# Performance work log

Measured on AMD Instinct MI355X. Metric: run time of the kernel, lower is better.

Reference implementation:

```python
import jax, jax.numpy as jnp
import numpy as np

H = 128
STEPS = 4
EPS = 1e-5

def _mlp(x, W0, b0, W1, b1, W2, b2):
    x = jax.nn.relu(x @ W0 + b0)
    x = jax.nn.relu(x @ W1 + b1)
    return x @ W2 + b2

def _ln(x, g, b):
    mu = jnp.mean(x, axis=-1, keepdims=True)
    var = jnp.mean((x - mu) ** 2, axis=-1, keepdims=True)
    return (x - mu) * jax.lax.rsqrt(var + EPS) * g + b

def _scores(x, pos):
    # soft assignment of points to graph nodes: softmax over -squared distance
    d2 = (jnp.sum(x * x, -1, keepdims=True)
          - 2.0 * jnp.einsum('bnd,md->bnm', x, pos)
          + jnp.sum(pos * pos, -1))  # [B, Npts, Nnodes]
    return jax.nn.softmax(-d2, axis=-1)

def _block(nodes, senders, receivers, msg_W, msg_b, ln1_g, ln1_b, node_W, node_b, ln2_g, ln2_b):
    # gather edge endpoints, message MLP, layernorm
    m = jnp.concatenate((nodes[:, receivers], nodes[:, senders]), axis=-1) @ msg_W + msg_b
    m = _ln(m, ln1_g, ln1_b)  # [B, E, H]
    inbox = jnp.zeros_like(nodes).at[:, receivers].add(m)  # scatter-add
    out = jnp.concatenate((nodes, inbox), axis=-1) @ node_W + node_b
    return _ln(out, ln2_g, ln2_b)

def setup_inputs() -> dict:
    key = jax.random.key(0)
    ks = jax.random.split(key, 40)
    B, Nc, Nt, N, E = 8, 4096, 4096, 1024, 16384
    dx, dyc, dyt = 2, 3, 3
    def w(k, *s):
        fan_in = s[0]
        return jax.random.normal(k, s, jnp.float32) / np.sqrt(fan_in)
    inp = {
        'xc': jax.random.normal(ks[0], (B, Nc, dx), jnp.float32),
        'yc': jax.random.normal(ks[1], (B, Nc, dyc), jnp.float32),
        'xt': jax.random.normal(ks[2], (B, Nt, dx), jnp.float32),
        'pos': jax.random.normal(ks[3], (N, dx), jnp.float32),
        'enc_W0': w(ks[4], dx + dyc, H), 'enc_b0': jnp.zeros((H,), jnp.float32),
        'enc_W1': w(ks[5], H, H), 'enc_b1': jnp.zeros((H,), jnp.float32),
        'enc_W2': w(ks[6], H, H), 'enc_b2': jnp.zeros((H,), jnp.float32),
        'qenc_W0': w(ks[7], dx, H), 'qenc_b0': jnp.zeros((H,), jnp.float32),
        'qenc_W1': w(ks[8], H, H), 'qenc_b1': jnp.zeros((H,), jnp.float32),
        'qenc_W2': w(ks[9], H, H), 'qenc_b2': jnp.zeros((H,), jnp.float32),
        'dec_W0': w(ks[10], 2 * H, H), 'dec_b0': jnp.zeros((H,), jnp.float32),
        'dec_W1': w(ks[11], H, H), 'dec_b1': jnp.zeros((H,), jnp.float32),
        'dec_W2': w(ks[12], H, dyt), 'dec_b2': jnp.zeros((dyt,), jnp.float32),
        'msg_W': w(ks[13], 2 * H, H), 'msg_b': jnp.zeros((H,), jnp.float32),
        'ln1_g': jnp.ones((H,), jnp.float32), 'ln1_b': jnp.zeros((H,), jnp.float32),
        'node_W': w(ks[14], 2 * H, H), 'node_b': jnp.zeros((H,), jnp.float32),
        'ln2_g': jnp.ones((H,), jnp.float32), 'ln2_b': jnp.zeros((H,), jnp.float32),
        'senders': jax.random.randint(ks[15], (E,), 0, N, jnp.int32),
        'receivers': jax.random.randint(ks[16], (E,), 0, N, jnp.int32),
    }
    return inp

def reference(xc, yc, xt, pos,
              enc_W0, enc_b0, enc_W1, enc_b1, enc_W2, enc_b2,
              qenc_W0, qenc_b0, qenc_W1, qenc_b1, qenc_W2, qenc_b2,
              dec_W0, dec_b0, dec_W1, dec_b1, dec_W2, dec_b2,
              msg_W, msg_b, ln1_g, ln1_b, node_W, node_b, ln2_g, ln2_b,
              senders, receivers):
    sc = _scores(xc, pos)  # [B, Nc, N]
    emb = _mlp(jnp.concatenate((xc, yc), -1), enc_W0, enc_b0, enc_W1, enc_b1, enc_W2, enc_b2)
    latents = jnp.einsum('bcn,bch->bnh', sc, emb)  # scores^T @ emb -> [B, N, H]
    for _ in range(STEPS):  # shared block (same weights each step)
        latents = _block(latents, senders, receivers, msg_W, msg_b, ln1_g, ln1_b,
                         node_W, node_b, ln2_g, ln2_b)
    q = _mlp(xt, qenc_W0, qenc_b0, qenc_W1, qenc_b1, qenc_W2, qenc_b2)
    st = _scores(xt, pos)  # [B, Nt, N]
    z = jnp.einsum('btn,bnh->bth', st, latents)
    z = jnp.concatenate((z, q), -1)
    return _mlp(z, dec_W0, dec_b0, dec_W1, dec_b1, dec_W2, dec_b2)
```

## Files before the change

### kernel.cpp

```cpp
#include <hip/hip_runtime.h>
#include <hip/hip_bf16.h>
#include <string.h>

#define BB 8
#define NC 4096
#define NTT 4096
#define NNODE 1024
#define NEDGE 16384
#define LDE 4128
#define LDL 1056

typedef __hip_bfloat16 bf16;
typedef unsigned short u16;
typedef __attribute__((ext_vector_type(8))) short short8;
typedef __attribute__((ext_vector_type(4))) float f32x4;

__device__ __forceinline__ float b2f(bf16 x) { return __bfloat162float(x); }
__device__ __forceinline__ float bs2f(short s) { return __uint_as_float(((unsigned)(unsigned short)s) << 16); }

template <typename T> struct Cvt;
template <> struct Cvt<float> { static __device__ __forceinline__ float to(float v) { return v; } };
template <> struct Cvt<bf16>  { static __device__ __forceinline__ bf16  to(float v) { return __float2bfloat16(v); } };

__device__ __forceinline__ unsigned short f2bs(float x) {
    unsigned u = __float_as_uint(x);
    return (unsigned short)((u + 0x7FFFu + ((u >> 16) & 1u)) >> 16);
}

__device__ __forceinline__ short8 ld_frag(const bf16* g) {
    union { uint4 u4; short8 s8; } cv;
    cv.u4 = *(const uint4*)g;
    return cv.s8;
}
__device__ __forceinline__ short8 ld_frag(const float* g) {
    float4 f0 = *(const float4*)g;
    float4 f1 = *(const float4*)(g + 4);
    short8 r;
    r[0] = (short)f2bs(f0.x); r[1] = (short)f2bs(f0.y);
    r[2] = (short)f2bs(f0.z); r[3] = (short)f2bs(f0.w);
    r[4] = (short)f2bs(f1.x); r[5] = (short)f2bs(f1.y);
    r[6] = (short)f2bs(f1.z); r[7] = (short)f2bs(f1.w);
    return r;
}

__global__ void detect_k(const u16* __restrict__ posu, int* __restrict__ flag) {
    __shared__ int cnt;
    if (threadIdx.x == 0) cnt = 0;
    __syncthreads();
    int wild = 0;
    for (int i = threadIdx.x; i < 1024; i += 256) {
        u16 u = posu[2 * i];
        int ex = (u >> 7) & 0xFF;
        if (ex == 0 || ex == 0xFF || ex > 137 || ex < 107) wild++;
    }
    atomicAdd(&cnt, wild);
    __syncthreads();
    if (threadIdx.x == 0) *flag = (cnt > 50) ? 1 : 0;
}

struct Tab { const void* src[30]; int pref[31]; };

__global__ __launch_bounds__(256) void ingest_k(Tab tab, const int* __restrict__ flag,
                                                bf16* __restrict__ dst) {
    int idx = blockIdx.x * 256 + threadIdx.x;
    if (idx >= tab.pref[30]) return;
    int t = 0;
    while (tab.pref[t + 1] <= idx) t++;
    int e = idx - tab.pref[t];
    float v;
    if (*flag) v = ((const float*)tab.src[t])[e];
    else       v = b2f(((const bf16*)tab.src[t])[e]);
    dst[idx] = __float2bfloat16(v);
}

struct TT { const bf16* src[11]; bf16* dst[11]; int srcK[11]; int dK[11]; int pref[12]; };

__global__ __launch_bounds__(256) void prep_trans_k(
    TT tt,
    const bf16* __restrict__ xc, const bf16* __restrict__ yc,
    const bf16* __restrict__ xt,
    const bf16* __restrict__ pos,
    bf16* __restrict__ xin32, bf16* __restrict__ xt32,
    float2* __restrict__ posf2) {
    if (blockIdx.x < 128) {
        int row = blockIdx.x * 256 + threadIdx.x;
        bf16 z = __float2bfloat16(0.f);
        bf16* xr = xin32 + row * 32;
        xr[0] = xc[row * 2 + 0];
        xr[1] = xc[row * 2 + 1];
        xr[2] = yc[row * 3 + 0];
        xr[3] = yc[row * 3 + 1];
        xr[4] = yc[row * 3 + 2];
#pragma unroll
        for (int k = 5; k < 32; ++k) xr[k] = z;
        bf16* tr = xt32 + row * 32;
        tr[0] = xt[row * 2 + 0];
        tr[1] = xt[row * 2 + 1];
#pragma unroll
        for (int k = 2; k < 32; ++k) tr[k] = z;
        if (row < NNODE) posf2[row] = make_float2(b2f(pos[2 * row]), b2f(pos[2 * row + 1]));
        return;
    }
    int idx = (blockIdx.x - 128) * 256 + threadIdx.x;
    if (idx >= tt.pref[11]) return;
    int t = 0;
    while (tt.pref[t + 1] <= idx) t++;
    int e = idx - tt.pref[t];
    int k = e >> 7, n = e & 127;
    bf16 v = (k < tt.srcK[t]) ? tt.src[t][k * 128 + n] : __float2bfloat16(0.f);
    tt.dst[t][n * tt.dK[t] + k] = v;
}

__global__ __launch_bounds__(1024) void build_csr_k(const int* __restrict__ recv,
                                                    const int* __restrict__ send,
                                                    int* __restrict__ rowptr,
                                                    int* __restrict__ csr_send) {
    __shared__ int cnt[1024];
    __shared__ int wt[16], wt2[16];
    __shared__ int cur[1024];
    int t = threadIdx.x;
    cnt[t] = 0;
    __syncthreads();
    for (int e = t; e < NEDGE; e += 1024) atomicAdd(&cnt[recv[e]], 1);
    __syncthreads();
    int v = cnt[t];
    int lane = t & 63, w = t >> 6;
#pragma unroll
    for (int off = 1; off < 64; off <<= 1) {
        int u = __shfl_up(v, off);
        if (lane >= off) v += u;
    }
    if (lane == 63) wt[w] = v;
    __syncthreads();
    if (t < 16) {
        int x = wt[t];
#pragma unroll
        for (int off = 1; off < 16; off <<= 1) {
            int u = __shfl_up(x, off);
            if (t >= off) x += u;
        }
        wt2[t] = x;
    }
    __syncthreads();
    int excl = v - cnt[t] + (w ? wt2[w - 1] : 0);
    rowptr[t] = excl;
    cur[t] = excl;
    if (t == 0) rowptr[1024] = NEDGE;
    __syncthreads();
    for (int e = t; e < NEDGE; e += 1024) {
        int pos = atomicAdd(&cur[recv[e]], 1);
        csr_send[pos] = send[e];
    }
}

template <int KSTEPS, int EPI, int RELU, int TRANS, int NSPLIT,
          typename TINA, typename TINB, typename TOUT>
__global__ __launch_bounds__(256) void mfma_gemm_k(
    const TINA* __restrict__ Xa, const TINB* __restrict__ Xb, int ldx,
    const bf16* __restrict__ Wt,
    const bf16* __restrict__ bias,
    const bf16* __restrict__ lng, const bf16* __restrict__ lnb,
    TOUT* __restrict__ Y, int ldy, int tshift, int ldt)
{
    constexpr int K = KSTEPS * 32;
    __shared__ __align__(16) short Bs[8][64][8];
    int tid = threadIdx.x;
    int w = tid >> 6, l = tid & 63;
    int lm = l & 15, lq = l >> 4;
    int blk = blockIdx.x;
    int half = 0;
    if (NSPLIT == 2) { half = blk & 1; blk >>= 1; }
    const bf16* Wtl = Wt + (size_t)half * 128 * K;
    int colbase = half * 128;
    size_t row0 = (size_t)blk * 64;

    f32x4 acc[8];
#pragma unroll
    for (int i = 0; i < 8; i++) acc[i] = (f32x4){0.f, 0.f, 0.f, 0.f};

    for (int s = 0; s < KSTEPS; ++s) {
        int k0 = s * 32;
        __syncthreads();
        short8 a;
        if (Xb != nullptr && k0 >= 128)
            a = ld_frag(Xb + (row0 + w * 16 + lm) * (size_t)128 + (k0 - 128) + lq * 8);
        else
            a = ld_frag(Xa + (row0 + w * 16 + lm) * (size_t)ldx + k0 + lq * 8);
#pragma unroll
        for (int rr = 0; rr < 2; ++rr) {
            int idx = rr * 256 + tid;
            int nt = idx >> 6, ll = idx & 63;
            *(short8*)&Bs[nt][ll][0] =
                ld_frag(Wtl + (size_t)(nt * 16 + (ll & 15)) * K + k0 + (ll >> 4) * 8);
        }
        __syncthreads();
#pragma unroll
        for (int nt = 0; nt < 8; ++nt) {
            short8 b = *(const short8*)&Bs[nt][l][0];
            acc[nt] = __builtin_amdgcn_mfma_f32_16x16x32_bf16(a, b, acc[nt], 0, 0, 0);
        }
    }

    float v[8][4];
#pragma unroll
    for (int nt = 0; nt < 8; ++nt) {
        float bb = bias ? b2f(bias[colbase + nt * 16 + lm]) : 0.f;
#pragma unroll
        for (int r = 0; r < 4; ++r) v[nt][r] = acc[nt][r] + bb;
    }
    if constexpr (EPI == 1) {
#pragma unroll
        for (int r = 0; r < 4; ++r) {
            float s1 = 0.f, s2 = 0.f;
#pragma unroll
            for (int nt = 0; nt < 8; ++nt) { s1 += v[nt][r]; s2 += v[nt][r] * v[nt][r]; }
#pragma unroll
            for (int m = 1; m < 16; m <<= 1) { s1 += __shfl_xor(s1, m); s2 += __shfl_xor(s2, m); }
            float mu = s1 * (1.f / 128.f);
            float var = s2 * (1.f / 128.f) - mu * mu;
            float rs = rsqrtf(var + 1e-5f);
#pragma unroll
            for (int nt = 0; nt < 8; ++nt) {
                int n = nt * 16 + lm;
                v[nt][r] = (v[nt][r] - mu) * rs * b2f(lng[n]) + b2f(lnb[n]);
            }
        }
    }
    if constexpr (TRANS) {
        size_t grow = row0 + w * 16 + lq * 4;
        int bb2 = (int)(grow >> tshift);
        size_t rloc = grow & (((size_t)1 << tshift) - 1);
        bf16* YT = (bf16*)Y;
#pragma unroll
        for (int nt = 0; nt < 8; ++nt) {
            int col = colbase + nt * 16 + lm;
            ushort4 u;
            float x0 = v[nt][0], x1 = v[nt][1], x2 = v[nt][2], x3 = v[nt][3];
            if (RELU) { x0 = fmaxf(x0, 0.f); x1 = fmaxf(x1, 0.f); x2 = fmaxf(x2, 0.f); x3 = fmaxf(x3, 0.f); }
            u.x = f2bs(x0); u.y = f2bs(x1); u.z = f2bs(x2); u.w = f2bs(x3);
            *(ushort4*)(YT + ((size_t)bb2 * 128 + col) * (size_t)ldt + rloc) = u;
        }
    } else {
#pragma unroll
        for (int nt = 0; nt < 8; ++nt)
#pragma unroll
            for (int r = 0; r < 4; ++r) {
                float x = v[nt][r];
                if (RELU) x = fmaxf(x, 0.f);
                Y[(row0 + w * 16 + lq * 4 + r) * (size_t)ldy + colbase + nt * 16 + lm] = Cvt<TOUT>::to(x);
            }
    }
}

__global__ __launch_bounds__(256) void node_msg_k(
    const float* __restrict__ cur, const bf16* __restrict__ inbox,
    const bf16* __restrict__ WtNode, const bf16* __restrict__ node_b,
    const bf16* __restrict__ ln2_g, const bf16* __restrict__ ln2_b,
    const bf16* __restrict__ WtMsg,
    float* __restrict__ nxt, bf16* __restrict__ PQ)
{
    __shared__ __align__(16) short Bs[8][64][8];
    __shared__ __align__(16) short Act[64][136];
    int tid = threadIdx.x;
    int w = tid >> 6, l = tid & 63;
    int lm = l & 15, lq = l >> 4;
    size_t row0 = (size_t)blockIdx.x * 64;

    f32x4 acc[8];
#pragma unroll
    for (int i = 0; i < 8; i++) acc[i] = (f32x4){0.f, 0.f, 0.f, 0.f};

    for (int s = 0; s < 8; ++s) {
        int k0 = s * 32;
        __syncthreads();
        short8 a;
        if (k0 < 128) a = ld_frag(cur + (row0 + w * 16 + lm) * 128 + k0 + lq * 8);
        else          a = ld_frag(inbox + (row0 + w * 16 + lm) * 128 + (k0 - 128) + lq * 8);
#pragma unroll
        for (int rr = 0; rr < 2; ++rr) {
            int idx = rr * 256 + tid;
            int nt = idx >> 6, ll = idx & 63;
            *(short8*)&Bs[nt][ll][0] =
                ld_frag(WtNode + (size_t)(nt * 16 + (ll & 15)) * 256 + k0 + (ll >> 4) * 8);
        }
        __syncthreads();
#pragma unroll
        for (int nt = 0; nt < 8; ++nt) {
            short8 b = *(const short8*)&Bs[nt][l][0];
            acc[nt] = __builtin_amdgcn_mfma_f32_16x16x32_bf16(a, b, acc[nt], 0, 0, 0);
        }
    }
    float v[8][4];
#pragma unroll
    for (int nt = 0; nt < 8; ++nt) {
        float bb = b2f(node_b[nt * 16 + lm]);
#pragma unroll
        for (int r = 0; r < 4; ++r) v[nt][r] = acc[nt][r] + bb;
    }
#pragma unroll
    for (int r = 0; r < 4; ++r) {
        float s1 = 0.f, s2 = 0.f;
#pragma unroll
        for (int nt = 0; nt < 8; ++nt) { s1 += v[nt][r]; s2 += v[nt][r] * v[nt][r]; }
#pragma unroll
        for (int m = 1; m < 16; m <<= 1) { s1 += __shfl_xor(s1, m); s2 += __shfl_xor(s2, m); }
        float mu = s1 * (1.f / 128.f);
        float var = s2 * (1.f / 128.f) - mu * mu;
        float rs = rsqrtf(var + 1e-5f);
#pragma unroll
        for (int nt = 0; nt < 8; ++nt) {
            int n = nt * 16 + lm;
            v[nt][r] = (v[nt][r] - mu) * rs * b2f(ln2_g[n]) + b2f(ln2_b[n]);
        }
    }
#pragma unroll
    for (int nt = 0; nt < 8; ++nt)
#pragma unroll
        for (int r = 0; r < 4; ++r) {
            nxt[(row0 + w * 16 + lq * 4 + r) * 128 + nt * 16 + lm] = v[nt][r];
            Act[w * 16 + lq * 4 + r][nt * 16 + lm] = (short)f2bs(v[nt][r]);
        }

    for (int half = 0; half < 2; ++half) {
        const bf16* Wtl = WtMsg + (size_t)half * 128 * 128;
#pragma unroll
        for (int i = 0; i < 8; i++) acc[i] = (f32x4){0.f, 0.f, 0.f, 0.f};
        for (int s = 0; s < 4; ++s) {
            int k0 = s * 32;
            __syncthreads();
#pragma unroll
            for (int rr = 0; rr < 2; ++rr) {
                int idx = rr * 256 + tid;
                int nt = idx >> 6, ll = idx & 63;
                *(short8*)&Bs[nt][ll][0] =
                    ld_frag(Wtl + (size_t)(nt * 16 + (ll & 15)) * 128 + k0 + (ll >> 4) * 8);
            }
            __syncthreads();
            short8 a = *(const short8*)&Act[w * 16 + lm][k0 + lq * 8];
#pragma unroll
            for (int nt = 0; nt < 8; ++nt) {
                short8 b = *(const short8*)&Bs[nt][l][0];
                acc[nt] = __builtin_amdgcn_mfma_f32_16x16x32_bf16(a, b, acc[nt], 0, 0, 0);
            }
        }
#pragma unroll
        for (int nt = 0; nt < 8; ++nt)
#pragma unroll
            for (int r = 0; r < 4; ++r)
                PQ[(row0 + w * 16 + lq * 4 + r) * 256 + half * 128 + nt * 16 + lm] =
                    __float2bfloat16(acc[nt][r]);
    }
}

template <int K0STEPS, int LAYERS, int RELU_LAST, int TRANS, typename TIN, typename TOUT>
__global__ __launch_bounds__(256) void mlp_k(
    const TIN* __restrict__ Xa, const TIN* __restrict__ Xb, int ldx,
    const bf16* __restrict__ Wt0, const bf16* __restrict__ b0,
    const bf16* __restrict__ Wt1, const bf16* __restrict__ b1,
    const bf16* __restrict__ Wt2, const bf16* __restrict__ b2,
    TOUT* __restrict__ Y, int ldy, int tshift, int ldt)
{
    constexpr int K0 = K0STEPS * 32;
    __shared__ __align__(16) short Bs[8][64][8];
    __shared__ __align__(16) short Act[64][136];
    int tid = threadIdx.x;
    int w = tid >> 6, l = tid & 63;
    int lm = l & 15, lq = l >> 4;
    size_t row0 = (size_t)blockIdx.x * 64;

    f32x4 acc[8];
#pragma unroll
    for (int i = 0; i < 8; i++) acc[i] = (f32x4){0.f, 0.f, 0.f, 0.f};

    for (int s = 0; s < K0STEPS; ++s) {
        int k0 = s * 32;
        __syncthreads();
        short8 a;
        {
            const TIN* src = Xa; int kk = k0; int ld = ldx;
            if (Xb != nullptr && k0 >= 128) { src = Xb; kk = k0 - 128; ld = 128; }
            a = ld_frag(src + (row0 + w * 16 + lm) * (size_t)ld + kk + lq * 8);
        }
#pragma unroll
        for (int rr = 0; rr < 2; ++rr) {
            int idx = rr * 256 + tid;
            int nt = idx >> 6, ll = idx & 63;
            *(short8*)&Bs[nt][ll][0] =
                ld_frag(Wt0 + (size_t)(nt * 16 + (ll & 15)) * K0 + k0 + (ll >> 4) * 8);
        }
        __syncthreads();
#pragma unroll
        for (int nt = 0; nt < 8; ++nt) {
            short8 b = *(const short8*)&Bs[nt][l][0];
            acc[nt] = __builtin_amdgcn_mfma_f32_16x16x32_bf16(a, b, acc[nt], 0, 0, 0);
        }
    }
#pragma unroll
    for (int nt = 0; nt < 8; ++nt) {
        float bb = b2f(b0[nt * 16 + lm]);
#pragma unroll
        for (int r = 0; r < 4; ++r) {
            float x = fmaxf(acc[nt][r] + bb, 0.f);
            Act[w * 16 + lq * 4 + r][nt * 16 + lm] = (short)f2bs(x);
        }
    }

    for (int L = 1; L < LAYERS; ++L) {
        const bf16* Wt = (L == 1) ? Wt1 : Wt2;
        const bf16* bias = (L == 1) ? b1 : b2;
        bool last = (L == LAYERS - 1);
#pragma unroll
        for (int i = 0; i < 8; i++) acc[i] = (f32x4){0.f, 0.f, 0.f, 0.f};
        for (int s = 0; s < 4; ++s) {
            int k0 = s * 32;
            __syncthreads();
#pragma unroll
            for (int rr = 0; rr < 2; ++rr) {
                int idx = rr * 256 + tid;
                int nt = idx >> 6, ll = idx & 63;
                *(short8*)&Bs[nt][ll][0] =
                    ld_frag(Wt + (size_t)(nt * 16 + (ll & 15)) * 128 + k0 + (ll >> 4) * 8);
            }
            __syncthreads();
            short8 a = *(const short8*)&Act[w * 16 + lm][k0 + lq * 8];
#pragma unroll
            for (int nt = 0; nt < 8; ++nt) {
                short8 b = *(const short8*)&Bs[nt][l][0];
                acc[nt] = __builtin_amdgcn_mfma_f32_16x16x32_bf16(a, b, acc[nt], 0, 0, 0);
            }
        }
        if (!last) {
            __syncthreads();
#pragma unroll
            for (int nt = 0; nt < 8; ++nt) {
                float bb = b2f(bias[nt * 16 + lm]);
#pragma unroll
                for (int r = 0; r < 4; ++r) {
                    float x = fmaxf(acc[nt][r] + bb, 0.f);
                    Act[w * 16 + lq * 4 + r][nt * 16 + lm] = (short)f2bs(x);
                }
            }
        } else {
            float v[8][4];
#pragma unroll
            for (int nt = 0; nt < 8; ++nt) {
                float bb = b2f(bias[nt * 16 + lm]);
#pragma unroll
                for (int r = 0; r < 4; ++r) {
                    float x = acc[nt][r] + bb;
                    if (RELU_LAST) x = fmaxf(x, 0.f);
                    v[nt][r] = x;
                }
            }
            if constexpr (TRANS) {
                size_t grow = row0 + w * 16 + lq * 4;
                int bb2 = (int)(grow >> tshift);
                size_t rloc = grow & (((size_t)1 << tshift) - 1);
                bf16* YT = (bf16*)Y;
#pragma unroll
                for (int nt = 0; nt < 8; ++nt) {
                    int col = nt * 16 + lm;
                    ushort4 u;
                    u.x = f2bs(v[nt][0]); u.y = f2bs(v[nt][1]);
                    u.z = f2bs(v[nt][2]); u.w = f2bs(v[nt][3]);
                    *(ushort4*)(YT + ((size_t)bb2 * 128 + col) * (size_t)ldt + rloc) = u;
                }
            } else {
#pragma unroll
                for (int nt = 0; nt < 8; ++nt)
#pragma unroll
                    for (int r = 0; r < 4; ++r)
                        Y[(row0 + w * 16 + lq * 4 + r) * (size_t)ldy + nt * 16 + lm] =
                            Cvt<TOUT>::to(v[nt][r]);
            }
        }
    }
}

__global__ __launch_bounds__(256) void qdec_k(
    const bf16* __restrict__ xt32,
    const bf16* __restrict__ WtQ0, const bf16* __restrict__ qb0,
    const bf16* __restrict__ WtQ1, const bf16* __restrict__ qb1,
    const bf16* __restrict__ WtQ2, const bf16* __restrict__ qb2,
    const bf16* __restrict__ z,
    const bf16* __restrict__ WtDec0, const bf16* __restrict__ db0,
    const bf16* __restrict__ WtDec1, const bf16* __restrict__ db1,
    const bf16* __restrict__ W2, const bf16* __restrict__ b2v,
    const int* __restrict__ flag, void* __restrict__ out)
{
    __shared__ __align__(16) short Bs[8][64][8];
    __shared__ __align__(16) short Act[64][136];
    __shared__ bf16 w2s[384];
    int tid = threadIdx.x;
    int w = tid >> 6, l = tid & 63;
    int lm = l & 15, lq = l >> 4;
    size_t row0 = (size_t)blockIdx.x * 64;
    for (int t = tid; t < 384; t += 256) w2s[t] = W2[t];

    f32x4 acc[8];
#pragma unroll
    for (int i = 0; i < 8; i++) acc[i] = (f32x4){0.f, 0.f, 0.f, 0.f};

    {
        __syncthreads();
#pragma unroll
        for (int rr = 0; rr < 2; ++rr) {
            int idx = rr * 256 + tid;
            int nt = idx >> 6, ll = idx & 63;
            *(short8*)&Bs[nt][ll][0] =
                ld_frag(WtQ0 + (size_t)(nt * 16 + (ll & 15)) * 32 + (ll >> 4) * 8);
        }
        __syncthreads();
        short8 a = ld_frag(xt32 + (row0 + w * 16 + lm) * 32 + lq * 8);
#pragma unroll
        for (int nt = 0; nt < 8; ++nt) {
            short8 b = *(const short8*)&Bs[nt][l][0];
            acc[nt] = __builtin_amdgcn_mfma_f32_16x16x32_bf16(a, b, acc[nt], 0, 0, 0);
        }
#pragma unroll
        for (int nt = 0; nt < 8; ++nt) {
            float bb = b2f(qb0[nt * 16 + lm]);
#pragma unroll
            for (int r = 0; r < 4; ++r)
                Act[w * 16 + lq * 4 + r][nt * 16 + lm] = (short)f2bs(fmaxf(acc[nt][r] + bb, 0.f));
        }
    }
    for (int L = 1; L < 3; ++L) {
        const bf16* Wt = (L == 1) ? WtQ1 : WtQ2;
        const bf16* bias = (L == 1) ? qb1 : qb2;
#pragma unroll
        for (int i = 0; i < 8; i++) acc[i] = (f32x4){0.f, 0.f, 0.f, 0.f};
        for (int s = 0; s < 4; ++s) {
            int k0 = s * 32;
            __syncthreads();
#pragma unroll
            for (int rr = 0; rr < 2; ++rr) {
                int idx = rr * 256 + tid;
                int nt = idx >> 6, ll = idx & 63;
                *(short8*)&Bs[nt][ll][0] =
                    ld_frag(Wt + (size_t)(nt * 16 + (ll & 15)) * 128 + k0 + (ll >> 4) * 8);
            }
            __syncthreads();
            short8 a = *(const short8*)&Act[w * 16 + lm][k0 + lq * 8];
#pragma unroll
            for (int nt = 0; nt < 8; ++nt) {
                short8 b = *(const short8*)&Bs[nt][l][0];
                acc[nt] = __builtin_amdgcn_mfma_f32_16x16x32_bf16(a, b, acc[nt], 0, 0, 0);
            }
        }
        __syncthreads();
#pragma unroll
        for (int nt = 0; nt < 8; ++nt) {
            float bb = b2f(bias[nt * 16 + lm]);
#pragma unroll
            for (int r = 0; r < 4; ++r) {
                float x = acc[nt][r] + bb;
                if (L == 1) x = fmaxf(x, 0.f);
                Act[w * 16 + lq * 4 + r][nt * 16 + lm] = (short)f2bs(x);
            }
        }
    }
    {
#pragma unroll
        for (int i = 0; i < 8; i++) acc[i] = (f32x4){0.f, 0.f, 0.f, 0.f};
        for (int s = 0; s < 8; ++s) {
            int k0 = s * 32;
            __syncthreads();
#pragma unroll
            for (int rr = 0; rr < 2; ++rr) {
                int idx = rr * 256 + tid;
                int nt = idx >> 6, ll = idx & 63;
                *(short8*)&Bs[nt][ll][0] =
                    ld_frag(WtDec0 + (size_t)(nt * 16 + (ll & 15)) * 256 + k0 + (ll >> 4) * 8);
            }
            __syncthreads();
            short8 a;
            if (k0 < 128) a = ld_frag(z + (row0 + w * 16 + lm) * (size_t)128 + k0 + lq * 8);
            else          a = *(const short8*)&Act[w * 16 + lm][(k0 - 128) + lq * 8];
#pragma unroll
            for (int nt = 0; nt < 8; ++nt) {
                short8 b = *(const short8*)&Bs[nt][l][0];
                acc[nt] = __builtin_amdgcn_mfma_f32_16x16x32_bf16(a, b, acc[nt], 0, 0, 0);
            }
        }
        __syncthreads();
#pragma unroll
        for (int nt = 0; nt < 8; ++nt) {
            float bb = b2f(db0[nt * 16 + lm]);
#pragma unroll
            for (int r = 0; r < 4; ++r)
                Act[w * 16 + lq * 4 + r][nt * 16 + lm] = (short)f2bs(fmaxf(acc[nt][r] + bb, 0.f));
        }
    }
    {
#pragma unroll
        for (int i = 0; i < 8; i++) acc[i] = (f32x4){0.f, 0.f, 0.f, 0.f};
        for (int s = 0; s < 4; ++s) {
            int k0 = s * 32;
            __syncthreads();
#pragma unroll
            for (int rr = 0; rr < 2; ++rr) {
                int idx = rr * 256 + tid;
                int nt = idx >> 6, ll = idx & 63;
                *(short8*)&Bs[nt][ll][0] =
                    ld_frag(WtDec1 + (size_t)(nt * 16 + (ll & 15)) * 128 + k0 + (ll >> 4) * 8);
            }
            __syncthreads();
            short8 a = *(const short8*)&Act[w * 16 + lm][k0 + lq * 8];
#pragma unroll
            for (int nt = 0; nt < 8; ++nt) {
                short8 b = *(const short8*)&Bs[nt][l][0];
                acc[nt] = __builtin_amdgcn_mfma_f32_16x16x32_bf16(a, b, acc[nt], 0, 0, 0);
            }
        }
        __syncthreads();
#pragma unroll
        for (int nt = 0; nt < 8; ++nt) {
            float bb = b2f(db1[nt * 16 + lm]);
#pragma unroll
            for (int r = 0; r < 4; ++r)
                Act[w * 16 + lq * 4 + r][nt * 16 + lm] = (short)f2bs(fmaxf(acc[nt][r] + bb, 0.f));
        }
    }
    __syncthreads();
    if (tid < 192) {
        int row = tid / 3, col = tid - (tid / 3) * 3;
        float a = b2f(b2v[col]);
        for (int k8 = 0; k8 < 16; ++k8) {
            short8 av = *(const short8*)&Act[row][k8 * 8];
#pragma unroll
            for (int j = 0; j < 8; ++j)
                a += bs2f(av[j]) * b2f(w2s[(k8 * 8 + j) * 3 + col]);
        }
        size_t o = (row0 + row) * 3 + col;
        if (*flag) ((float*)out)[o] = a;
        else       ((bf16*)out)[o] = __float2bfloat16(a);
    }
}

__global__ __launch_bounds__(256) void stats2_k(const bf16* __restrict__ xcp,
                                                const bf16* __restrict__ xtp,
                                                const bf16* __restrict__ pos,
                                                float4* __restrict__ cstC4,
                                                float4* __restrict__ cstT4) {
    __shared__ float px[NNODE], py[NNODE];
    int tid = threadIdx.x;
    for (int t = tid; t < NNODE; t += 256) {
        px[t] = b2f(pos[2 * t]);
        py[t] = b2f(pos[2 * t + 1]);
    }
    __syncthreads();
    const bf16* xp = (blockIdx.x < 8192) ? xcp : xtp;
    float4* st4 = (blockIdx.x < 8192) ? cstC4 : cstT4;
    int pb = blockIdx.x & 8191;
    int w = tid >> 6, l = tid & 63;
    int p = pb * 4 + w;
    float x = b2f(xp[2 * p]), y = b2f(xp[2 * p + 1]);
    float vals[16];
    float m = -3.4e38f;
#pragma unroll
    for (int k = 0; k < 16; k++) {
        int n = k * 64 + l;
        float dx = x - px[n], dy = y - py[n];
        float v = -(dx * dx + dy * dy);
        vals[k] = v;
        m = fmaxf(m, v);
    }
#pragma unroll
    for (int off = 32; off; off >>= 1) m = fmaxf(m, __shfl_xor(m, off));
    float s = 0.f;
#pragma unroll
    for (int k = 0; k < 16; k++) s += __expf(vals[k] - m);
#pragma unroll
    for (int off = 32; off; off >>= 1) s += __shfl_xor(s, off);
    if (l == 0) st4[p] = make_float4(x, y, m, 1.f / s);
}

struct P8 { float* p[8]; };

__global__ __launch_bounds__(512, 4) void lat_mfma_k(const bf16* __restrict__ embT,
                                                     const float2* __restrict__ posf2,
                                                     const float4* __restrict__ cstC4,
                                                     P8 parts) {
    int i = blockIdx.x;
    int b = i & 7, r = i >> 3;
    int cs = r >> 4, nt = r & 15;
    int n0 = nt * 64;
    __shared__ __align__(16) float4 csh[512];
    __shared__ __align__(16) float4 red[4][8][64];
    int tid = threadIdx.x;
    int w = tid >> 6, l = tid & 63;
    int wl = w & 3, up = w >> 2;
    int lm = l & 15, lq = l >> 4;
    int node = n0 + wl * 16 + lm;
    float2 pn = posf2[node];
    const bf16* ebase = embT + (size_t)b * (128 * LDE) + cs * 512;
    const float4* cbase = cstC4 + b * NC + cs * 512;
    for (int t = tid; t < 512; t += 512) csh[t] = cbase[t];
    __syncthreads();

    f32x4 acc[8];
#pragma unroll
    for (int q = 0; q < 8; q++) acc[q] = (f32x4){0.f, 0.f, 0.f, 0.f};

    union AF { short8 s; u16 u[8]; };
    AF cw, nw;
    short8 bc[8], bn[8];
    int chb = up * 8;
    int c00 = chb * 32;
#pragma unroll
    for (int j = 0; j < 8; ++j) {
        float4 cc = csh[c00 + lq * 8 + j];
        float dx = cc.x - pn.x, dy = cc.y - pn.y;
        cw.u[j] = f2bs(__expf(-(dx * dx + dy * dy) - cc.z) * cc.w);
    }
#pragma unroll
    for (int t2 = 0; t2 < 8; ++t2)
        bc[t2] = ld_frag(ebase + (size_t)(t2 * 16 + lm) * LDE + c00 + lq * 8);

    for (int ch = 0; ch < 8; ++ch) {
        int c0n = (chb + ((ch + 1) & 7)) * 32;
#pragma unroll
        for (int t2 = 0; t2 < 8; ++t2)
            bn[t2] = ld_frag(ebase + (size_t)(t2 * 16 + lm) * LDE + c0n + lq * 8);
#pragma unroll
        for (int j = 0; j < 8; ++j) {
            float4 cc = csh[c0n + lq * 8 + j];
            float dx = cc.x - pn.x, dy = cc.y - pn.y;
            nw.u[j] = f2bs(__expf(-(dx * dx + dy * dy) - cc.z) * cc.w);
        }
#pragma unroll
        for (int t2 = 0; t2 < 8; ++t2)
            acc[t2] = __builtin_amdgcn_mfma_f32_16x16x32_bf16(cw.s, bc[t2], acc[t2], 0, 0, 0);
        cw = nw;
#pragma unroll
        for (int t2 = 0; t2 < 8; ++t2) bc[t2] = bn[t2];
    }
    if (up) {
#pragma unroll
        for (int t2 = 0; t2 < 8; ++t2)
            red[wl][t2][l] = make_float4(acc[t2][0], acc[t2][1], acc[t2][2], acc[t2][3]);
    }
    __syncthreads();
    if (!up) {
        float* part = parts.p[cs] + (((size_t)(b * NNODE + n0 + wl * 16 + lq * 4)) << 7) + lm;
#pragma unroll
        for (int t2 = 0; t2 < 8; ++t2) {
            float4 o = red[wl][t2][l];
#pragma unroll
            for (int r2 = 0; r2 < 4; ++r2)
                part[(r2 << 7) + t2 * 16] = acc[t2][r2] + ((const float*)&o)[r2];
        }
    }
}

__global__ __launch_bounds__(256) void reduce8_k(float* __restrict__ dst, P8 parts) {
    int i = blockIdx.x * 256 + threadIdx.x;
    float4 s = ((const float4*)parts.p[0])[i];
#pragma unroll
    for (int k = 1; k < 8; ++k) {
        float4 v = ((const float4*)parts.p[k])[i];
        s.x += v.x; s.y += v.y; s.z += v.z; s.w += v.w;
    }
    ((float4*)dst)[i] = s;
}

__global__ __launch_bounds__(512, 4) void z_mfma_k(const bf16* __restrict__ latT,
                                                   const float2* __restrict__ posf2,
                                                   const float4* __restrict__ cstT4,
                                                   bf16* __restrict__ z) {
    int i = blockIdx.x;
    int b = i & 7, tt = i >> 3;
    int t0 = tt * 64;
    __shared__ __align__(8) float2 posh[1024];
    __shared__ __align__(16) float4 red[4][8][64];
    int tid = threadIdx.x;
    int w = tid >> 6, l = tid & 63;
    int wl = w & 3, up = w >> 2;
    int lm = l & 15, lq = l >> 4;
    int t = t0 + wl * 16 + lm;
    float4 qs = cstT4[b * NTT + t];
    const bf16* lbase = latT + (size_t)b * (128 * LDL);
    for (int k = tid; k < 1024; k += 512) posh[k] = posf2[k];
    __syncthreads();

    f32x4 acc[8];
#pragma unroll
    for (int q = 0; q < 8; q++) acc[q] = (f32x4){0.f, 0.f, 0.f, 0.f};

    union AF { short8 s; u16 u[8]; };
    AF cw, nw;
    short8 bc[8], bn[8];
    int chb = up * 16;
    int nb0 = chb * 32;
#pragma unroll
    for (int j = 0; j < 8; ++j) {
        float2 pn = posh[nb0 + lq * 8 + j];
        float dx = qs.x - pn.x, dy = qs.y - pn.y;
        cw.u[j] = f2bs(__expf(-(dx * dx + dy * dy) - qs.z) * qs.w);
    }
#pragma unroll
    for (int t2 = 0; t2 < 8; ++t2)
        bc[t2] = ld_frag(lbase + (size_t)(t2 * 16 + lm) * LDL + nb0 + lq * 8);

    for (int ch = 0; ch < 16; ++ch) {
        int nbn = (chb + ((ch + 1) & 15)) * 32;
#pragma unroll
        for (int t2 = 0; t2 < 8; ++t2)
            bn[t2] = ld_frag(lbase + (size_t)(t2 * 16 + lm) * LDL + nbn + lq * 8);
#pragma unroll
        for (int j = 0; j < 8; ++j) {
            float2 pn = posh[nbn + lq * 8 + j];
            float dx = qs.x - pn.x, dy = qs.y - pn.y;
            nw.u[j] = f2bs(__expf(-(dx * dx + dy * dy) - qs.z) * qs.w);
        }
#pragma unroll
        for (int t2 = 0; t2 < 8; ++t2)
            acc[t2] = __builtin_amdgcn_mfma_f32_16x16x32_bf16(cw.s, bc[t2], acc[t2], 0, 0, 0);
        cw = nw;
#pragma unroll
        for (int t2 = 0; t2 < 8; ++t2) bc[t2] = bn[t2];
    }
    if (up) {
#pragma unroll
        for (int t2 = 0; t2 < 8; ++t2)
            red[wl][t2][l] = make_float4(acc[t2][0], acc[t2][1], acc[t2][2], acc[t2][3]);
    }
    __syncthreads();
    if (!up) {
        bf16* zp = z + (((size_t)(b * NTT + t0 + wl * 16 + lq * 4)) << 7) + lm;
#pragma unroll
        for (int t2 = 0; t2 < 8; ++t2) {
            float4 o = red[wl][t2][l];
#pragma unroll
            for (int r2 = 0; r2 < 4; ++r2)
                zp[(r2 << 7) + t2 * 16] = __float2bfloat16(acc[t2][r2] + ((const float*)&o)[r2]);
        }
    }
}

__global__ __launch_bounds__(256) void edge_gather_k(const bf16* __restrict__ PQ,
                                                     const int* __restrict__ rowptr,
                                                     const int* __restrict__ csr_send,
                                                     const bf16* __restrict__ mb,
                                                     const bf16* __restrict__ g1,
                                                     const bf16* __restrict__ b1,
                                                     bf16* __restrict__ inbox) {
    int tid = threadIdx.x;
    int w = tid >> 6, l = tid & 63;
    int gw = blockIdx.x * 4 + w;
    int b = gw >> 10, n = gw & 1023;
    const bf16* pqb = PQ + ((size_t)b << 18);
    float p0 = b2f(pqb[(n << 8) + l]);
    float p1 = b2f(pqb[(n << 8) + l + 64]);
    float mb0 = b2f(mb[l]), mb1 = b2f(mb[l + 64]);
    float g0 = b2f(g1[l]), g1v = b2f(g1[l + 64]);
    float bb0 = b2f(b1[l]), bb1 = b2f(b1[l + 64]);
    int beg = rowptr[n], end = rowptr[n + 1];
    float a0 = 0.f, a1 = 0.f;
    int i = beg;
    for (; i + 1 < end; i += 2) {
        int sA = csr_send[i], sB = csr_send[i + 1];
        const bf16* qA = pqb + (sA << 8) + 128;
        const bf16* qB = pqb + (sB << 8) + 128;
        float A0 = p0 + b2f(qA[l]) + mb0;
        float A1 = p1 + b2f(qA[l + 64]) + mb1;
        float B0 = p0 + b2f(qB[l]) + mb0;
        float B1 = p1 + b2f(qB[l + 64]) + mb1;
        float a1s = A0 + A1, a2s = A0 * A0 + A1 * A1;
        float b1s = B0 + B1, b2s = B0 * B0 + B1 * B1;
#pragma unroll
        for (int off = 32; off; off >>= 1) {
            a1s += __shfl_xor(a1s, off);
            a2s += __shfl_xor(a2s, off);
            b1s += __shfl_xor(b1s, off);
            b2s += __shfl_xor(b2s, off);
        }
        float muA = a1s * (1.f / 128.f);
        float varA = a2s * (1.f / 128.f) - muA * muA;
        float rsA = rsqrtf(varA + 1e-5f);
        float muB = b1s * (1.f / 128.f);
        float varB = b2s * (1.f / 128.f) - muB * muB;
        float rsB = rsqrtf(varB + 1e-5f);
        a0 += (A0 - muA) * rsA * g0 + bb0;
        a1 += (A1 - muA) * rsA * g1v + bb1;
        a0 += (B0 - muB) * rsB * g0 + bb0;
        a1 += (B1 - muB) * rsB * g1v + bb1;
    }
    if (i < end) {
        int s = csr_send[i];
        const bf16* q = pqb + (s << 8) + 128;
        float m0 = p0 + b2f(q[l]) + mb0;
        float m1 = p1 + b2f(q[l + 64]) + mb1;
        float s1 = m0 + m1, s2 = m0 * m0 + m1 * m1;
#pragma unroll
        for (int off = 32; off; off >>= 1) {
            s1 += __shfl_xor(s1, off);
            s2 += __shfl_xor(s2, off);
        }
        float mu = s1 * (1.f / 128.f);
        float var = s2 * (1.f / 128.f) - mu * mu;
        float rs = rsqrtf(var + 1e-5f);
        a0 += (m0 - mu) * rs * g0 + bb0;
        a1 += (m1 - mu) * rs * g1v + bb1;
    }
    bf16* inb = inbox + ((size_t)b << 17) + (n << 7);
    inb[l] = __float2bfloat16(a0);
    inb[l + 64] = __float2bfloat16(a1);
}

extern "C" void kernel_launch(void* const* d_in, const int* in_sizes, int n_in,
                              void* d_out, int out_size, void* d_ws, size_t ws_size,
                              hipStream_t stream) {
    const int* senders = (const int*)d_in[30];
    const int* receivers = (const int*)d_in[31];

    char* base = (char*)d_ws;
    size_t off = 0;
    auto alloc = [&](size_t bytes) { char* p = base + off; off += (bytes + 255) & ~(size_t)255; return p; };

    int* flag = (int*)alloc(256);

    Tab tab;
    int pref = 0;
    for (int i = 0; i < 30; ++i) { tab.src[i] = d_in[i]; tab.pref[i] = pref; pref += in_sizes[i]; }
    tab.pref[30] = pref;
    bf16* arena = (bf16*)alloc((size_t)pref * 2);
    auto C = [&](int i) { return arena + tab.pref[i]; };

    float4* cstC4 = (float4*)alloc(32768 * sizeof(float4));
    float4* cstT4 = (float4*)alloc(32768 * sizeof(float4));
    float* lat0  = (float*)alloc(8192 * 128 * 4);
    float* lat1  = (float*)alloc(8192 * 128 * 4);
    float* inboxf = (float*)alloc(8192 * 128 * 4);
    bf16* inbox  = (bf16*)alloc(8192 * 128 * 2);
    bf16* T1     = (bf16*)alloc((size_t)32768 * 128 * 2);
    bf16* T2     = (bf16*)alloc((size_t)32768 * 128 * 2);
    bf16* T3     = (bf16*)alloc((size_t)32768 * 128 * 2);
    bf16* embT   = (bf16*)alloc((size_t)8 * 128 * LDE * 2);
    bf16* latT   = (bf16*)alloc((size_t)8 * 128 * LDL * 2);
    bf16* xin32  = (bf16*)alloc((size_t)32768 * 32 * 2);
    bf16* xt32   = (bf16*)alloc((size_t)32768 * 32 * 2);
    float2* posf2 = (float2*)alloc(1024 * sizeof(float2));
    int* rowptr  = (int*)alloc(1025 * 4);
    int* csr_send = (int*)alloc(NEDGE * 4);
    bf16* WtEnc0 = (bf16*)alloc(128 * 32 * 2);
    bf16* WtQ0   = (bf16*)alloc(128 * 32 * 2);
    bf16* WtEnc1 = (bf16*)alloc(16384 * 2);
    bf16* WtEnc2 = (bf16*)alloc(16384 * 2);
    bf16* WtQ1   = (bf16*)alloc(16384 * 2);
    bf16* WtQ2   = (bf16*)alloc(16384 * 2);
    bf16* WtDec0 = (bf16*)alloc(32768 * 2);
    bf16* WtDec1 = (bf16*)alloc(16384 * 2);
    bf16* WtMsg  = (bf16*)alloc(32768 * 2);
    bf16* WtNode = (bf16*)alloc(32768 * 2);
    bf16* PQ     = T3;
    (void)ws_size; (void)n_in; (void)out_size;

    detect_k<<<1, 256, 0, stream>>>((const u16*)d_in[3], flag);
    ingest_k<<<(pref + 255) / 256, 256, 0, stream>>>(tab, flag, arena);

    const bf16 *xc = C(0), *yc = C(1), *xt = C(2), *pos = C(3);
    const bf16 *enc_W0 = C(4), *enc_b0 = C(5), *enc_W1 = C(6), *enc_b1 = C(7), *enc_W2 = C(8), *enc_b2 = C(9);
    const bf16 *qenc_W0 = C(10), *qenc_b0 = C(11), *qenc_W1 = C(12), *qenc_b1 = C(13), *qenc_W2 = C(14), *qenc_b2 = C(15);
    const bf16 *dec_W0 = C(16), *dec_b0 = C(17), *dec_W1 = C(18), *dec_b1 = C(19), *dec_W2 = C(20), *dec_b2 = C(21);
    const bf16 *msg_W = C(22), *msg_b = C(23), *ln1_g = C(24), *ln1_b = C(25);
    const bf16 *node_W = C(26), *node_b = C(27), *ln2_g = C(28), *ln2_b = C(29);

    TT tt;
    const bf16* s11[11] = { enc_W1, enc_W2, qenc_W1, qenc_W2, dec_W1, dec_W0, msg_W, msg_W + 16384, node_W, enc_W0, qenc_W0 };
    bf16* d11[11]       = { WtEnc1, WtEnc2, WtQ1,    WtQ2,    WtDec1, WtDec0, WtMsg, WtMsg + 16384, WtNode, WtEnc0, WtQ0   };
    int sk11[11] = { 128, 128, 128, 128, 128, 256, 128, 128, 256, 5, 2 };
    int dk11[11] = { 128, 128, 128, 128, 128, 256, 128, 128, 256, 32, 32 };
    int tp = 0;
    for (int i = 0; i < 11; ++i) {
        tt.src[i] = s11[i]; tt.dst[i] = d11[i]; tt.srcK[i] = sk11[i]; tt.dK[i] = dk11[i];
        tt.pref[i] = tp; tp += dk11[i] * 128;
    }
    tt.pref[11] = tp;

    prep_trans_k<<<128 + (tp + 255) / 256, 256, 0, stream>>>(tt, xc, yc, xt, pos, xin32, xt32, posf2);
    build_csr_k<<<1, 1024, 0, stream>>>(receivers, senders, rowptr, csr_send);

    mlp_k<1, 3, 0, 1, bf16, bf16><<<512, 256, 0, stream>>>(
        xin32, nullptr, 32, WtEnc0, enc_b0, WtEnc1, enc_b1, WtEnc2, enc_b2, embT, 128, 12, LDE);

    stats2_k<<<16384, 256, 0, stream>>>(xc, xt, pos, cstC4, cstT4);

    P8 parts;
    parts.p[0] = lat1;
    parts.p[1] = inboxf;
    parts.p[2] = (float*)T1;
    parts.p[3] = (float*)T1 + 1048576;
    parts.p[4] = (float*)T2;
    parts.p[5] = (float*)T2 + 1048576;
    parts.p[6] = (float*)T3;
    parts.p[7] = (float*)T3 + 1048576;
    lat_mfma_k<<<1024, 512, 0, stream>>>(embT, posf2, cstC4, parts);
    reduce8_k<<<1024, 256, 0, stream>>>(lat0, parts);

    mfma_gemm_k<4, 0, 0, 0, 2, float, float, bf16><<<256, 256, 0, stream>>>(lat0, nullptr, 128, WtMsg, nullptr, nullptr, nullptr, PQ, 256, 0, 0);
    edge_gather_k<<<2048, 256, 0, stream>>>(PQ, rowptr, csr_send, msg_b, ln1_g, ln1_b, inbox);
    node_msg_k<<<128, 256, 0, stream>>>(lat0, inbox, WtNode, node_b, ln2_g, ln2_b, WtMsg, lat1, PQ);
    edge_gather_k<<<2048, 256, 0, stream>>>(PQ, rowptr, csr_send, msg_b, ln1_g, ln1_b, inbox);
    node_msg_k<<<128, 256, 0, stream>>>(lat1, inbox, WtNode, node_b, ln2_g, ln2_b, WtMsg, lat0, PQ);
    edge_gather_k<<<2048, 256, 0, stream>>>(PQ, rowptr, csr_send, msg_b, ln1_g, ln1_b, inbox);
    node_msg_k<<<128, 256, 0, stream>>>(lat0, inbox, WtNode, node_b, ln2_g, ln2_b, WtMsg, lat1, PQ);
    edge_gather_k<<<2048, 256, 0, stream>>>(PQ, rowptr, csr_send, msg_b, ln1_g, ln1_b, inbox);
    mfma_gemm_k<8, 1, 0, 1, 1, float, bf16, bf16><<<128, 256, 0, stream>>>(lat1, inbox, 128, WtNode, node_b, ln2_g, ln2_b, latT, 128, 10, LDL);

    z_mfma_k<<<512, 512, 0, stream>>>(latT, posf2, cstT4, T2);

    qdec_k<<<512, 256, 0, stream>>>(xt32,
                                    WtQ0, qenc_b0, WtQ1, qenc_b1, WtQ2, qenc_b2,
                                    T2,
                                    WtDec0, dec_b0, WtDec1, dec_b1,
                                    dec_W2, dec_b2, flag, d_out);
}
```

Measured before the change: 478.6 us.

## Stage B fragments through double-buffered swizzled LDS in lat and z MFMA kernels

```diff
diff --git a/kernel.cpp b/kernel.cpp
--- a/kernel.cpp
+++ b/kernel.cpp
@@ -687,7 +687,10 @@
     int cs = r >> 4, nt = r & 15;
     int n0 = nt * 64;
     __shared__ __align__(16) float4 csh[512];
-    __shared__ __align__(16) float4 red[4][8][64];
+    __shared__ __align__(16) union ShU {
+        short stage[2][8192];
+        float4 red[4][8][64];
+    } sh;
     int tid = threadIdx.x;
     int w = tid >> 6, l = tid & 63;
     int wl = w & 3, up = w >> 2;
@@ -696,7 +699,22 @@
     float2 pn = posf2[node];
     const bf16* ebase = embT + (size_t)b * (128 * LDE) + cs * 512;
     const float4* cbase = cstC4 + b * NC + cs * 512;
-    for (int t = tid; t < 512; t += 512) csh[t] = cbase[t];
+    csh[tid] = cbase[tid];
+
+    int h0 = tid >> 3;
+    int cb0 = (tid & 7) << 4;
+    const char* g0 = (const char*)ebase + (size_t)h0 * (LDE * 2) + cb0;
+    const size_t gH = (size_t)64 * (LDE * 2);
+    int o0 = h0 * 128 + (cb0 ^ ((h0 & 7) << 4));
+    char* lbuf0 = (char*)&sh.stage[0][0];
+    char* lbuf1 = (char*)&sh.stage[1][0];
+
+    {
+        uint4 rA = *(const uint4*)(g0);
+        uint4 rB = *(const uint4*)(g0 + gH);
+        *(uint4*)(lbuf0 + o0) = rA;
+        *(uint4*)(lbuf0 + o0 + 64 * 128) = rB;
+    }
     __syncthreads();
 
     f32x4 acc[8];
@@ -704,49 +722,49 @@
     for (int q = 0; q < 8; q++) acc[q] = (f32x4){0.f, 0.f, 0.f, 0.f};
 
     union AF { short8 s; u16 u[8]; };
-    AF cw, nw;
-    short8 bc[8], bn[8];
-    int chb = up * 8;
-    int c00 = chb * 32;
-#pragma unroll
-    for (int j = 0; j < 8; ++j) {
-        float4 cc = csh[c00 + lq * 8 + j];
-        float dx = cc.x - pn.x, dy = cc.y - pn.y;
-        cw.u[j] = f2bs(__expf(-(dx * dx + dy * dy) - cc.z) * cc.w);
-    }
-#pragma unroll
-    for (int t2 = 0; t2 < 8; ++t2)
-        bc[t2] = ld_frag(ebase + (size_t)(t2 * 16 + lm) * LDE + c00 + lq * 8);
-
-    for (int ch = 0; ch < 8; ++ch) {
-        int c0n = (chb + ((ch + 1) & 7)) * 32;
+    int rb = up * 64 + lq * 16;
+
+    for (int ci = 0; ci < 8; ++ci) {
+        char* cur = (ci & 1) ? lbuf1 : lbuf0;
+        char* nxt = (ci & 1) ? lbuf0 : lbuf1;
+        uint4 rA, rB;
+        if (ci < 7) {
+            const char* gs = g0 + (ci + 1) * 128;
+            rA = *(const uint4*)(gs);
+            rB = *(const uint4*)(gs + gH);
+        }
+        AF cw;
+        int cidx = ci * 64 + up * 32 + lq * 8;
+#pragma unroll
+        for (int j = 0; j < 8; ++j) {
+            float4 cc = csh[cidx + j];
+            float dx = cc.x - pn.x, dy = cc.y - pn.y;
+            cw.u[j] = f2bs(__expf(-(dx * dx + dy * dy) - cc.z) * cc.w);
+        }
+#pragma unroll
+        for (int t2 = 0; t2 < 8; ++t2) {
+            int h = t2 * 16 + lm;
+            short8 bfr = *(const short8*)(cur + h * 128 + (rb ^ ((h & 7) << 4)));
+            acc[t2] = __builtin_amdgcn_mfma_f32_16x16x32_bf16(cw.s, bfr, acc[t2], 0, 0, 0);
+        }
+        if (ci < 7) {
+            *(uint4*)(nxt + o0) = rA;
+            *(uint4*)(nxt + o0 + 64 * 128) = rB;
+        }
+        __syncthreads();
+    }
+
+    if (up) {
 #pragma unroll
         for (int t2 = 0; t2 < 8; ++t2)
-            bn[t2] = ld_frag(ebase + (size_t)(t2 * 16 + lm) * LDE + c0n + lq * 8);
-#pragma unroll
-        for (int j = 0; j < 8; ++j) {
-            float4 cc = csh[c0n + lq * 8 + j];
-            float dx = cc.x - pn.x, dy = cc.y - pn.y;
-            nw.u[j] = f2bs(__expf(-(dx * dx + dy * dy) - cc.z) * cc.w);
-        }
-#pragma unroll
-        for (int t2 = 0; t2 < 8; ++t2)
-            acc[t2] = __builtin_amdgcn_mfma_f32_16x16x32_bf16(cw.s, bc[t2], acc[t2], 0, 0, 0);
-        cw = nw;
-#pragma unroll
-        for (int t2 = 0; t2 < 8; ++t2) bc[t2] = bn[t2];
-    }
-    if (up) {
-#pragma unroll
-        for (int t2 = 0; t2 < 8; ++t2)
-            red[wl][t2][l] = make_float4(acc[t2][0], acc[t2][1], acc[t2][2], acc[t2][3]);
+            sh.red[wl][t2][l] = make_float4(acc[t2][0], acc[t2][1], acc[t2][2], acc[t2][3]);
     }
     __syncthreads();
     if (!up) {
         float* part = parts.p[cs] + (((size_t)(b * NNODE + n0 + wl * 16 + lq * 4)) << 7) + lm;
 #pragma unroll
         for (int t2 = 0; t2 < 8; ++t2) {
-            float4 o = red[wl][t2][l];
+            float4 o = sh.red[wl][t2][l];
 #pragma unroll
             for (int r2 = 0; r2 < 4; ++r2)
                 part[(r2 << 7) + t2 * 16] = acc[t2][r2] + ((const float*)&o)[r2];
@@ -773,7 +791,10 @@
     int b = i & 7, tt = i >> 3;
     int t0 = tt * 64;
     __shared__ __align__(8) float2 posh[1024];
-    __shared__ __align__(16) float4 red[4][8][64];
+    __shared__ __align__(16) union ShU {
+        short stage[2][8192];
+        float4 red[4][8][64];
+    } sh;
     int tid = threadIdx.x;
     int w = tid >> 6, l = tid & 63;
     int wl = w & 3, up = w >> 2;
@@ -782,6 +803,21 @@
     float4 qs = cstT4[b * NTT + t];
     const bf16* lbase = latT + (size_t)b * (128 * LDL);
     for (int k = tid; k < 1024; k += 512) posh[k] = posf2[k];
+
+    int h0 = tid >> 3;
+    int cb0 = (tid & 7) << 4;
+    const char* g0 = (const char*)lbase + (size_t)h0 * (LDL * 2) + cb0;
+    const size_t gH = (size_t)64 * (LDL * 2);
+    int o0 = h0 * 128 + (cb0 ^ ((h0 & 7) << 4));
+    char* lbuf0 = (char*)&sh.stage[0][0];
+    char* lbuf1 = (char*)&sh.stage[1][0];
+
+    {
+        uint4 rA = *(const uint4*)(g0);
+        uint4 rB = *(const uint4*)(g0 + gH);
+        *(uint4*)(lbuf0 + o0) = rA;
+        *(uint4*)(lbuf0 + o0 + 64 * 128) = rB;
+    }
     __syncthreads();
 
     f32x4 acc[8];
@@ -789,49 +825,49 @@
     for (int q = 0; q < 8; q++) acc[q] = (f32x4){0.f, 0.f, 0.f, 0.f};
 
     union AF { short8 s; u16 u[8]; };
-    AF cw, nw;
-    short8 bc[8], bn[8];
-    int chb = up * 16;
-    int nb0 = chb * 32;
-#pragma unroll
-    for (int j = 0; j < 8; ++j) {
-        float2 pn = posh[nb0 + lq * 8 + j];
-        float dx = qs.x - pn.x, dy = qs.y - pn.y;
-        cw.u[j] = f2bs(__expf(-(dx * dx + dy * dy) - qs.z) * qs.w);
-    }
-#pragma unroll
-    for (int t2 = 0; t2 < 8; ++t2)
-        bc[t2] = ld_frag(lbase + (size_t)(t2 * 16 + lm) * LDL + nb0 + lq * 8);
-
-    for (int ch = 0; ch < 16; ++ch) {
-        int nbn = (chb + ((ch + 1) & 15)) * 32;
+    int rb = up * 64 + lq * 16;
+
+    for (int ci = 0; ci < 16; ++ci) {
+        char* cur = (ci & 1) ? lbuf1 : lbuf0;
+        char* nxt = (ci & 1) ? lbuf0 : lbuf1;
+        uint4 rA, rB;
+        if (ci < 15) {
+            const char* gs = g0 + (ci + 1) * 128;
+            rA = *(const uint4*)(gs);
+            rB = *(const uint4*)(gs + gH);
+        }
+        AF cw;
+        int cidx = ci * 64 + up * 32 + lq * 8;
+#pragma unroll
+        for (int j = 0; j < 8; ++j) {
+            float2 pn = posh[cidx + j];
+            float dx = qs.x - pn.x, dy = qs.y - pn.y;
+            cw.u[j] = f2bs(__expf(-(dx * dx + dy * dy) - qs.z) * qs.w);
+        }
+#pragma unroll
+        for (int t2 = 0; t2 < 8; ++t2) {
+            int h = t2 * 16 + lm;
+            short8 bfr = *(const short8*)(cur + h * 128 + (rb ^ ((h & 7) << 4)));
+            acc[t2] = __builtin_amdgcn_mfma_f32_16x16x32_bf16(cw.s, bfr, acc[t2], 0, 0, 0);
+        }
+        if (ci < 15) {
+            *(uint4*)(nxt + o0) = rA;
+            *(uint4*)(nxt + o0 + 64 * 128) = rB;
+        }
+        __syncthreads();
+    }
+
+    if (up) {
 #pragma unroll
         for (int t2 = 0; t2 < 8; ++t2)
-            bn[t2] = ld_frag(lbase + (size_t)(t2 * 16 + lm) * LDL + nbn + lq * 8);
-#pragma unroll
-        for (int j = 0; j < 8; ++j) {
-            float2 pn = posh[nbn + lq * 8 + j];
-            float dx = qs.x - pn.x, dy = qs.y - pn.y;
-            nw.u[j] = f2bs(__expf(-(dx * dx + dy * dy) - qs.z) * qs.w);
-        }
-#pragma unroll
-        for (int t2 = 0; t2 < 8; ++t2)
-            acc[t2] = __builtin_amdgcn_mfma_f32_16x16x32_bf16(cw.s, bc[t2], acc[t2], 0, 0, 0);
-        cw = nw;
-#pragma unroll
-        for (int t2 = 0; t2 < 8; ++t2) bc[t2] = bn[t2];
-    }
-    if (up) {
-#pragma unroll
-        for (int t2 = 0; t2 < 8; ++t2)
-            red[wl][t2][l] = make_float4(acc[t2][0], acc[t2][1], acc[t2][2], acc[t2][3]);
+            sh.red[wl][t2][l] = make_float4(acc[t2][0], acc[t2][1], acc[t2][2], acc[t2][3]);
     }
     __syncthreads();
     if (!up) {
         bf16* zp = z + (((size_t)(b * NTT + t0 + wl * 16 + lq * 4)) << 7) + lm;
 #pragma unroll
         for (int t2 = 0; t2 < 8; ++t2) {
-            float4 o = red[wl][t2][l];
+            float4 o = sh.red[wl][t2][l];
 #pragma unroll
             for (int r2 = 0; r2 < 4; ++r2)
                 zp[(r2 << 7) + t2 * 16] = __float2bfloat16(acc[t2][r2] + ((const float*)&o)[r2]);
```

After: 442.1 us. 7.6% less time.
